# Performance work log

Measured on AMD Instinct MI355X. Metric: run time of the kernel, lower is better.

The kernel has to match this reference:

```python
import jax, jax.numpy as jnp
import numpy as np

N_ITERS = 10
ETA = 0.1


def setup_inputs() -> dict:
    key = jax.random.key(0)
    k1, k2, k3 = jax.random.split(key, 3)
    u = jax.random.normal(k1, (65536, 512), dtype=jnp.float32)
    G_raw = jax.random.normal(k2, (512, 512), dtype=jnp.float32) * 0.01
    # log_lam initialized as log(0.5), matching lam_init=0.5
    log_lam = jnp.asarray(np.log(0.5), dtype=jnp.float32)
    return {"u": u, "G_raw": G_raw, "log_lam": log_lam}


def reference(u, G_raw, log_lam):
    lam = jnp.exp(log_lam)
    # symmetrize and zero the diagonal
    G = 0.5 * (G_raw + G_raw.T)
    G = G - jnp.diag(jnp.diagonal(G))

    def step(carry, _):
        v, a = carry
        dv = u - v - a @ G          # [N, dim]
        v = v + ETA * dv
        a = jnp.sign(v) * jax.nn.relu(jnp.abs(v) - lam)  # soft threshold
        return (v, a), None

    init = (jnp.zeros_like(u), jnp.zeros_like(u))
    (v, a), _ = jax.lax.scan(step, init, None, length=N_ITERS)
    return a
```

## Files before the change

kernel.cpp:

```cpp
#include <hip/hip_runtime.h>
#include <hip/hip_bf16.h>


typedef __attribute__((ext_vector_type(8))) short bf16x8;
typedef __attribute__((ext_vector_type(16))) float f32x16;

#define ETA 0.1f

__device__ __forceinline__ unsigned short f2bf(float f) {
  union { float f; unsigned u; } x; x.f = f;
  unsigned r = x.u + 0x7fffu + ((x.u >> 16) & 1u);
  return (unsigned short)(r >> 16);
}

__global__ void prep_G(const float* __restrict__ Graw, unsigned short* __restrict__ Gb) {
  int idx = blockIdx.x * blockDim.x + threadIdx.x;
  int k = idx >> 9, n = idx & 511;
  float g = 0.5f * (Graw[k * 512 + n] + Graw[n * 512 + k]);
  if (k == n) g = 0.f;
  int kk = k >> 4, ct = n >> 5;
  int lane = (n & 31) + (((k >> 3) & 1) << 5);
  int j = k & 7;
  Gb[((((kk * 16 + ct) * 64) + lane) << 3) + j] = f2bf(g);
}

__global__ __launch_bounds__(512, 2) void lca_kernel(
    const float* __restrict__ u_g, const unsigned short* __restrict__ Gb,
    const float* __restrict__ log_lam, float* __restrict__ out) {
  __shared__ unsigned short sA[64 * 520];

  const int tid = threadIdx.x;
  const int lane = tid & 63;
  const int wave = tid >> 6;
  const int R0 = blockIdx.x * 64;
  const int cl = lane & 31;
  const int rquad = (lane >> 5) * 4;
  const int C0 = wave * 64;

  const float lam = expf(log_lam[0]);

  f32x16 acc[2][2];
  f32x16 uu[2][2];

  #pragma unroll
  for (int rt = 0; rt < 2; ++rt) {
    #pragma unroll
    for (int ctl = 0; ctl < 2; ++ctl) {
      const float* base = u_g + (R0 + rt * 32 + rquad) * 512 + C0 + ctl * 32 + cl;
      f32x16 t;
      #pragma unroll
      for (int reg = 0; reg < 16; ++reg) {
        const int rofs = (reg & 3) + 8 * (reg >> 2);
        t[reg] = base[rofs * 512];
      }
      uu[rt][ctl] = t;
      acc[rt][ctl] = -t;
    }
  }

  auto epilogue = [&]() {
    #pragma unroll
    for (int rt = 0; rt < 2; ++rt) {
      #pragma unroll
      for (int ctl = 0; ctl < 2; ++ctl) {
        unsigned short* sa = &sA[(rt * 32 + rquad) * 520 + C0 + ctl * 32 + cl];
        #pragma unroll
        for (int reg = 0; reg < 16; ++reg) {
          const int rofs = (reg & 3) + 8 * (reg >> 2);
          float v = -ETA * acc[rt][ctl][reg];
          float av = copysignf(fmaxf(fabsf(v) - lam, 0.f), v);
          sa[rofs * 520] = f2bf(av);
        }
        acc[rt][ctl] = 0.9f * acc[rt][ctl] - uu[rt][ctl];
      }
    }
  };

  epilogue();
  __syncthreads();

  const unsigned short* paRow = sA + cl * 520 + ((lane >> 5) << 3);
  const bf16x8* gb = (const bf16x8*)Gb;
  const int bbase = wave * 2 * 64 + lane;

  #pragma unroll 1
  for (int t = 1; t < 10; ++t) {
    #pragma unroll 4
    for (int kk = 0; kk < 32; ++kk) {
      bf16x8 a0 = *(const bf16x8*)(paRow + kk * 16);
      bf16x8 a1 = *(const bf16x8*)(paRow + 32 * 520 + kk * 16);
      bf16x8 b0 = gb[bbase + kk * 1024];
      bf16x8 b1 = gb[bbase + kk * 1024 + 64];
      acc[0][0] = __builtin_amdgcn_mfma_f32_32x32x16_bf16(a0, b0, acc[0][0], 0, 0, 0);
      acc[0][1] = __builtin_amdgcn_mfma_f32_32x32x16_bf16(a0, b1, acc[0][1], 0, 0, 0);
      acc[1][0] = __builtin_amdgcn_mfma_f32_32x32x16_bf16(a1, b0, acc[1][0], 0, 0, 0);
      acc[1][1] = __builtin_amdgcn_mfma_f32_32x32x16_bf16(a1, b1, acc[1][1], 0, 0, 0);
    }
    __syncthreads();
    if (t < 9) {
      epilogue();
      __syncthreads();
    }
  }

  #pragma unroll
  for (int rt = 0; rt < 2; ++rt) {
    #pragma unroll
    for (int ctl = 0; ctl < 2; ++ctl) {
      float* ob = out + (R0 + rt * 32 + rquad) * 512 + C0 + ctl * 32 + cl;
      #pragma unroll
      for (int reg = 0; reg < 16; ++reg) {
        const int rofs = (reg & 3) + 8 * (reg >> 2);
        float v = -ETA * acc[rt][ctl][reg];
        ob[rofs * 512] = copysignf(fmaxf(fabsf(v) - lam, 0.f), v);
      }
    }
  }
}

extern "C" void kernel_launch(void* const* d_in, const int* in_sizes, int n_in,
                              void* d_out, int out_size, void* d_ws, size_t ws_size,
                              hipStream_t stream) {
  const float* u = (const float*)d_in[0];
  const float* Graw = (const float*)d_in[1];
  const float* log_lam = (const float*)d_in[2];
  float* out = (float*)d_out;
  unsigned short* Gb = (unsigned short*)d_ws;

  prep_G<<<dim3(1024), dim3(256), 0, stream>>>(Graw, Gb);
  lca_kernel<<<dim3(1024), dim3(512), 0, stream>>>(u, Gb, log_lam, out);
}
```

Before: 538.6 us.

## Use 16 waves per block, double-buffer activations in LDS, stagger K start

Each block now runs 1024 threads (16 waves), and each wave owns 32 output columns instead of 64. This halves the accumulator registers per wave. The LDS activation tile is double-buffered, so one of the two barriers per iteration can be dropped: the epilogue writes the other buffer while slower waves may still be reading. The K-loop start is rotated per block group to spread global reads of the G matrix across different addresses. The trade-offs are twice the LDS per block, likely only one block per CU, and less B-operand reuse per wave.

```diff
diff --git a/kernel.cpp b/kernel.cpp
--- a/kernel.cpp
+++ b/kernel.cpp
@@ -24,10 +24,10 @@
   Gb[((((kk * 16 + ct) * 64) + lane) << 3) + j] = f2bf(g);
 }
 
-__global__ __launch_bounds__(512, 2) void lca_kernel(
+__global__ __launch_bounds__(1024) void lca_kernel(
     const float* __restrict__ u_g, const unsigned short* __restrict__ Gb,
     const float* __restrict__ log_lam, float* __restrict__ out) {
-  __shared__ unsigned short sA[64 * 520];
+  __shared__ unsigned short sA[2][64 * 520];
 
   const int tid = threadIdx.x;
   const int lane = tid & 63;
@@ -35,85 +35,74 @@
   const int R0 = blockIdx.x * 64;
   const int cl = lane & 31;
   const int rquad = (lane >> 5) * 4;
-  const int C0 = wave * 64;
+  const int C0 = wave * 32;
+  const int s = (blockIdx.x >> 3) & 31;
 
   const float lam = expf(log_lam[0]);
 
-  f32x16 acc[2][2];
-  f32x16 uu[2][2];
+  f32x16 acc[2];
+  f32x16 uu[2];
 
   #pragma unroll
   for (int rt = 0; rt < 2; ++rt) {
+    const float* base = u_g + (R0 + rt * 32 + rquad) * 512 + C0 + cl;
+    f32x16 t;
     #pragma unroll
-    for (int ctl = 0; ctl < 2; ++ctl) {
-      const float* base = u_g + (R0 + rt * 32 + rquad) * 512 + C0 + ctl * 32 + cl;
-      f32x16 t;
+    for (int reg = 0; reg < 16; ++reg) {
+      const int rofs = (reg & 3) + 8 * (reg >> 2);
+      t[reg] = base[rofs * 512];
+    }
+    uu[rt] = t;
+    acc[rt] = -t;
+  }
+
+  auto epilogue = [&](unsigned short* sbuf) {
+    #pragma unroll
+    for (int rt = 0; rt < 2; ++rt) {
+      unsigned short* sa = &sbuf[(rt * 32 + rquad) * 520 + C0 + cl];
       #pragma unroll
       for (int reg = 0; reg < 16; ++reg) {
         const int rofs = (reg & 3) + 8 * (reg >> 2);
-        t[reg] = base[rofs * 512];
+        float v = -ETA * acc[rt][reg];
+        float av = copysignf(fmaxf(fabsf(v) - lam, 0.f), v);
+        sa[rofs * 520] = f2bf(av);
       }
-      uu[rt][ctl] = t;
-      acc[rt][ctl] = -t;
-    }
-  }
-
-  auto epilogue = [&]() {
-    #pragma unroll
-    for (int rt = 0; rt < 2; ++rt) {
-      #pragma unroll
-      for (int ctl = 0; ctl < 2; ++ctl) {
-        unsigned short* sa = &sA[(rt * 32 + rquad) * 520 + C0 + ctl * 32 + cl];
-        #pragma unroll
-        for (int reg = 0; reg < 16; ++reg) {
-          const int rofs = (reg & 3) + 8 * (reg >> 2);
-          float v = -ETA * acc[rt][ctl][reg];
-          float av = copysignf(fmaxf(fabsf(v) - lam, 0.f), v);
-          sa[rofs * 520] = f2bf(av);
-        }
-        acc[rt][ctl] = 0.9f * acc[rt][ctl] - uu[rt][ctl];
-      }
+      acc[rt] = 0.9f * acc[rt] - uu[rt];
     }
   };
 
-  epilogue();
+  epilogue(sA[0]);
   __syncthreads();
 
-  const unsigned short* paRow = sA + cl * 520 + ((lane >> 5) << 3);
   const bf16x8* gb = (const bf16x8*)Gb;
-  const int bbase = wave * 2 * 64 + lane;
+  const int bbase = wave * 64 + lane;
 
   #pragma unroll 1
   for (int t = 1; t < 10; ++t) {
+    const unsigned short* paRow = sA[(t + 1) & 1] + cl * 520 + ((lane >> 5) << 3);
     #pragma unroll 4
     for (int kk = 0; kk < 32; ++kk) {
-      bf16x8 a0 = *(const bf16x8*)(paRow + kk * 16);
-      bf16x8 a1 = *(const bf16x8*)(paRow + 32 * 520 + kk * 16);
-      bf16x8 b0 = gb[bbase + kk * 1024];
-      bf16x8 b1 = gb[bbase + kk * 1024 + 64];
-      acc[0][0] = __builtin_amdgcn_mfma_f32_32x32x16_bf16(a0, b0, acc[0][0], 0, 0, 0);
-      acc[0][1] = __builtin_amdgcn_mfma_f32_32x32x16_bf16(a0, b1, acc[0][1], 0, 0, 0);
-      acc[1][0] = __builtin_amdgcn_mfma_f32_32x32x16_bf16(a1, b0, acc[1][0], 0, 0, 0);
-      acc[1][1] = __builtin_amdgcn_mfma_f32_32x32x16_bf16(a1, b1, acc[1][1], 0, 0, 0);
+      const int kko = (kk + s) & 31;
+      bf16x8 a0 = *(const bf16x8*)(paRow + kko * 16);
+      bf16x8 a1 = *(const bf16x8*)(paRow + 32 * 520 + kko * 16);
+      bf16x8 b0 = gb[bbase + kko * 1024];
+      acc[0] = __builtin_amdgcn_mfma_f32_32x32x16_bf16(a0, b0, acc[0], 0, 0, 0);
+      acc[1] = __builtin_amdgcn_mfma_f32_32x32x16_bf16(a1, b0, acc[1], 0, 0, 0);
     }
-    __syncthreads();
     if (t < 9) {
-      epilogue();
+      epilogue(sA[t & 1]);
       __syncthreads();
     }
   }
 
   #pragma unroll
   for (int rt = 0; rt < 2; ++rt) {
+    float* ob = out + (R0 + rt * 32 + rquad) * 512 + C0 + cl;
     #pragma unroll
-    for (int ctl = 0; ctl < 2; ++ctl) {
-      float* ob = out + (R0 + rt * 32 + rquad) * 512 + C0 + ctl * 32 + cl;
-      #pragma unroll
-      for (int reg = 0; reg < 16; ++reg) {
-        const int rofs = (reg & 3) + 8 * (reg >> 2);
-        float v = -ETA * acc[rt][ctl][reg];
-        ob[rofs * 512] = copysignf(fmaxf(fabsf(v) - lam, 0.f), v);
-      }
+    for (int reg = 0; reg < 16; ++reg) {
+      const int rofs = (reg & 3) + 8 * (reg >> 2);
+      float v = -ETA * acc[rt][reg];
+      ob[rofs * 512] = copysignf(fmaxf(fabsf(v) - lam, 0.f), v);
     }
   }
 }
@@ -128,5 +117,5 @@
   unsigned short* Gb = (unsigned short*)d_ws;
 
   prep_G<<<dim3(1024), dim3(256), 0, stream>>>(Graw, Gb);
-  lca_kernel<<<dim3(1024), dim3(512), 0, stream>>>(u, Gb, log_lam, out);
+  lca_kernel<<<dim3(1024), dim3(1024), 0, stream>>>(u, Gb, log_lam, out);
 }
```

Result: faster. 481.4 us (-10.6%).

## Double-buffer activation LDS, prefetch G fragments, stagger K start per block

Applied to the files above, without the earlier changes.

Activations in LDS are double-buffered, so each iteration's epilogue writes the other buffer and one barrier per iteration goes away. G fragments are held in registers and prefetched four K-steps ahead in a rotating scheme, which hides global or L2 latency behind the MFMAs. Each block group starts its K loop at a different offset to spread L2 accesses, and MFMA issue is wrapped in s_setprio. LDS use doubles (about 133KB per block), which may keep two 512-thread blocks from fitting on a CU, and the extra prefetch registers raise register pressure.

```diff
diff --git a/kernel.cpp b/kernel.cpp
--- a/kernel.cpp
+++ b/kernel.cpp
@@ -27,7 +27,7 @@
 __global__ __launch_bounds__(512, 2) void lca_kernel(
     const float* __restrict__ u_g, const unsigned short* __restrict__ Gb,
     const float* __restrict__ log_lam, float* __restrict__ out) {
-  __shared__ unsigned short sA[64 * 520];
+  __shared__ unsigned short sA[2][64 * 520];
 
   const int tid = threadIdx.x;
   const int lane = tid & 63;
@@ -36,6 +36,7 @@
   const int cl = lane & 31;
   const int rquad = (lane >> 5) * 4;
   const int C0 = wave * 64;
+  const int s = (blockIdx.x >> 3) & 31;
 
   const float lam = expf(log_lam[0]);
 
@@ -46,62 +47,84 @@
   for (int rt = 0; rt < 2; ++rt) {
     #pragma unroll
     for (int ctl = 0; ctl < 2; ++ctl) {
-      const float* base = u_g + (R0 + rt * 32 + rquad) * 512 + C0 + ctl * 32 + cl;
-      f32x16 t;
+      const int lrow = rt * 32 + rquad;
+      const int gcol = C0 + ctl * 32 + cl;
+      const float* ub = u_g + (R0 + lrow) * 512 + gcol;
+      unsigned short* sa = &sA[0][lrow * 520 + gcol];
       #pragma unroll
       for (int reg = 0; reg < 16; ++reg) {
         const int rofs = (reg & 3) + 8 * (reg >> 2);
-        t[reg] = base[rofs * 512];
+        float uv = ub[rofs * 512];
+        uu[rt][ctl][reg] = uv;
+        float v = ETA * uv;
+        float av = copysignf(fmaxf(fabsf(v) - lam, 0.f), v);
+        sa[rofs * 520] = f2bf(av);
+        acc[rt][ctl][reg] = -1.9f * uv;
       }
-      uu[rt][ctl] = t;
-      acc[rt][ctl] = -t;
     }
   }
 
-  auto epilogue = [&]() {
+  const bf16x8* gb = (const bf16x8*)Gb;
+  const int bb = (wave * 2) * 64 + lane;
+
+  bf16x8 p0a = gb[bb + ((s + 0) & 31) * 1024], p0b = gb[bb + ((s + 0) & 31) * 1024 + 64];
+  bf16x8 p1a = gb[bb + ((s + 1) & 31) * 1024], p1b = gb[bb + ((s + 1) & 31) * 1024 + 64];
+  bf16x8 p2a = gb[bb + ((s + 2) & 31) * 1024], p2b = gb[bb + ((s + 2) & 31) * 1024 + 64];
+  bf16x8 p3a = gb[bb + ((s + 3) & 31) * 1024], p3b = gb[bb + ((s + 3) & 31) * 1024 + 64];
+
+  __syncthreads();
+
+  auto epilogue = [&](unsigned short* sbuf) {
     #pragma unroll
     for (int rt = 0; rt < 2; ++rt) {
       #pragma unroll
       for (int ctl = 0; ctl < 2; ++ctl) {
-        unsigned short* sa = &sA[(rt * 32 + rquad) * 520 + C0 + ctl * 32 + cl];
+        unsigned short* sa = &sbuf[(rt * 32 + rquad) * 520 + C0 + ctl * 32 + cl];
         #pragma unroll
         for (int reg = 0; reg < 16; ++reg) {
           const int rofs = (reg & 3) + 8 * (reg >> 2);
           float v = -ETA * acc[rt][ctl][reg];
           float av = copysignf(fmaxf(fabsf(v) - lam, 0.f), v);
           sa[rofs * 520] = f2bf(av);
+          acc[rt][ctl][reg] = 0.9f * acc[rt][ctl][reg] - uu[rt][ctl][reg];
         }
-        acc[rt][ctl] = 0.9f * acc[rt][ctl] - uu[rt][ctl];
       }
     }
   };
 
-  epilogue();
-  __syncthreads();
-
-  const unsigned short* paRow = sA + cl * 520 + ((lane >> 5) << 3);
-  const bf16x8* gb = (const bf16x8*)Gb;
-  const int bbase = wave * 2 * 64 + lane;
+#define STEP(KBASE, J, PA, PB)                                                   \
+  do {                                                                           \
+    const int kc = ((KBASE) + (J) + s) & 31;                                     \
+    const int kl = ((KBASE) + (J) + 4 + s) & 31;                                 \
+    bf16x8 a0 = *(const bf16x8*)(paRow + kc * 16);                               \
+    bf16x8 a1 = *(const bf16x8*)(paRow + 32 * 520 + kc * 16);                    \
+    __builtin_amdgcn_s_setprio(1);                                               \
+    acc[0][0] = __builtin_amdgcn_mfma_f32_32x32x16_bf16(a0, PA, acc[0][0], 0, 0, 0); \
+    acc[0][1] = __builtin_amdgcn_mfma_f32_32x32x16_bf16(a0, PB, acc[0][1], 0, 0, 0); \
+    acc[1][0] = __builtin_amdgcn_mfma_f32_32x32x16_bf16(a1, PA, acc[1][0], 0, 0, 0); \
+    acc[1][1] = __builtin_amdgcn_mfma_f32_32x32x16_bf16(a1, PB, acc[1][1], 0, 0, 0); \
+    __builtin_amdgcn_s_setprio(0);                                               \
+    PA = gb[bb + kl * 1024];                                                     \
+    PB = gb[bb + kl * 1024 + 64];                                                \
+  } while (0)
 
   #pragma unroll 1
   for (int t = 1; t < 10; ++t) {
-    #pragma unroll 4
-    for (int kk = 0; kk < 32; ++kk) {
-      bf16x8 a0 = *(const bf16x8*)(paRow + kk * 16);
-      bf16x8 a1 = *(const bf16x8*)(paRow + 32 * 520 + kk * 16);
-      bf16x8 b0 = gb[bbase + kk * 1024];
-      bf16x8 b1 = gb[bbase + kk * 1024 + 64];
-      acc[0][0] = __builtin_amdgcn_mfma_f32_32x32x16_bf16(a0, b0, acc[0][0], 0, 0, 0);
-      acc[0][1] = __builtin_amdgcn_mfma_f32_32x32x16_bf16(a0, b1, acc[0][1], 0, 0, 0);
-      acc[1][0] = __builtin_amdgcn_mfma_f32_32x32x16_bf16(a1, b0, acc[1][0], 0, 0, 0);
-      acc[1][1] = __builtin_amdgcn_mfma_f32_32x32x16_bf16(a1, b1, acc[1][1], 0, 0, 0);
+    const unsigned short* paRow = sA[(t + 1) & 1] + cl * 520 + ((lane >> 5) << 3);
+    #pragma unroll 1
+    for (int grp = 0; grp < 8; ++grp) {
+      const int k4 = grp * 4;
+      STEP(k4, 0, p0a, p0b);
+      STEP(k4, 1, p1a, p1b);
+      STEP(k4, 2, p2a, p2b);
+      STEP(k4, 3, p3a, p3b);
     }
-    __syncthreads();
     if (t < 9) {
-      epilogue();
+      epilogue(sA[t & 1]);
       __syncthreads();
     }
   }
+#undef STEP
 
   #pragma unroll
   for (int rt = 0; rt < 2; ++rt) {
```

Result: faster. 476.6 us (-11.5%).
